# Performance work log

Hardware: AMD Instinct MI355X
Metric: run time of the kernel (lower is better)

Reference implementation:

```python
import jax, jax.numpy as jnp
import numpy as np

B, L, H, E = 4, 2048, 16, 64  # batch, seq, heads, head_dim (S=L, D=E)


def setup_inputs() -> dict:
    key = jax.random.key(0)
    kq, kk, kv = jax.random.split(key, 3)
    queries = jax.random.normal(kq, (B, L, H, E), dtype=jnp.float32)
    keys = jax.random.normal(kk, (B, L, H, E), dtype=jnp.float32)
    values = jax.random.normal(kv, (B, L, H, E), dtype=jnp.float32)
    return {"queries": queries, "keys": keys, "values": values}


def reference(queries, keys, values):
    Bq, Lq, Hq, Eq = queries.shape
    scale = 1.0 / float(np.sqrt(Eq))
    # scores: [B, H, L, S]
    scores = jnp.einsum('blhe,bshe->bhls', queries, keys)
    # causal mask: forbid attending to future positions (strict upper triangle)
    causal = jnp.triu(jnp.ones((Lq, Lq), dtype=bool), k=1)
    scores = jnp.where(causal[None, None, :, :], -jnp.inf, scores)
    A = jax.nn.softmax(scale * scores, axis=-1)  # dropout p=0 -> identity
    V = jnp.einsum('bhls,bshd->blhd', A, values)  # [B, L, H, D]
    return V
```

## Files before the change

kernel.cpp:

```cpp
#include <hip/hip_runtime.h>
#include <hip/hip_bf16.h>

typedef short bs8 __attribute__((ext_vector_type(8)));
typedef short bs4 __attribute__((ext_vector_type(4)));
typedef float f32x4 __attribute__((ext_vector_type(4)));
typedef float f32x16 __attribute__((ext_vector_type(16)));
typedef int i32x4 __attribute__((ext_vector_type(4)));

#define B_ 4
#define L_ 2048
#define H_ 16
#define E_ 64
#define KT_ 64
#define KSTR 72
#define SCSTR 68
#define NEG_INF (-1e30f)
#define SCALE_LOG2E (0.125f * 1.44269504088896340736f)

__device__ __forceinline__ short bf16of(float x) {
  __hip_bfloat16 h = __float2bfloat16(x);
  return *reinterpret_cast<short*>(&h);
}

__global__ __launch_bounds__(256) void prep(const float* __restrict__ K,
                                            const float* __restrict__ V,
                                            short* __restrict__ Kb,
                                            short* __restrict__ Vt) {
  __shared__ unsigned int lt[64 * 35];
  const int tid = threadIdx.x;
  if (blockIdx.x < 1024) {
    size_t base = (size_t)blockIdx.x * 256 + tid;
#pragma unroll
    for (int i = 0; i < 8; ++i) {
      size_t g = base + (size_t)i * 262144;
      int e4 = g & 15;
      int h  = (g >> 4) & 15;
      int s  = (g >> 8) & 2047;
      int b  = (int)(g >> 19);
      float4 v = *(const float4*)(K + g * 4);
      bs4 o;
      o.x = bf16of(v.x); o.y = bf16of(v.y); o.z = bf16of(v.z); o.w = bf16of(v.w);
      *(bs4*)(Kb + (((size_t)(b * 16 + h) * L_ + s) * E_ + e4 * 4)) = o;
    }
  } else {
    int vb = blockIdx.x - 1024;
    int st = vb & 31, bh = vb >> 5;
    int b = bh >> 4, h = bh & 15;
    int s0 = st * 64;
#pragma unroll
    for (int i = 0; i < 2; ++i) {
      int idx = i * 256 + tid;
      int sp = idx >> 4;
      int e4 = idx & 15;
      const float* p0 = V + (((size_t)b * L_ + s0 + 2 * sp) * H_ + h) * E_ + e4 * 4;
      float4 v0 = *(const float4*)p0;
      float4 v1 = *(const float4*)(p0 + H_ * E_);
      unsigned u;
      u = (unsigned short)bf16of(v0.x) | ((unsigned)(unsigned short)bf16of(v1.x) << 16);
      lt[(e4 * 4 + 0) * 35 + sp] = u;
      u = (unsigned short)bf16of(v0.y) | ((unsigned)(unsigned short)bf16of(v1.y) << 16);
      lt[(e4 * 4 + 1) * 35 + sp] = u;
      u = (unsigned short)bf16of(v0.z) | ((unsigned)(unsigned short)bf16of(v1.z) << 16);
      lt[(e4 * 4 + 2) * 35 + sp] = u;
      u = (unsigned short)bf16of(v0.w) | ((unsigned)(unsigned short)bf16of(v1.w) << 16);
      lt[(e4 * 4 + 3) * 35 + sp] = u;
    }
    __syncthreads();
#pragma unroll
    for (int i = 0; i < 2; ++i) {
      int idx = i * 256 + tid;
      int e  = idx >> 3;
      int s8 = idx & 7;
      uint4 o;
      o.x = lt[e * 35 + s8 * 4 + 0];
      o.y = lt[e * 35 + s8 * 4 + 1];
      o.z = lt[e * 35 + s8 * 4 + 2];
      o.w = lt[e * 35 + s8 * 4 + 3];
      *(uint4*)(Vt + ((size_t)bh * E_ + e) * L_ + s0 + 8 * s8) = o;
    }
  }
}

__global__ __launch_bounds__(256, 3) void flash_fwd(const float* __restrict__ Q,
                                                    const short* __restrict__ Kb,
                                                    const short* __restrict__ Vt,
                                                    float* __restrict__ O) {
  const int id  = blockIdx.x;
  const int xcd = id & 7;
  const int j   = id >> 3;
  const int qt  = 15 - (j & 15);
  const int bh  = xcd * 8 + (j >> 4);
  const int b = bh >> 4, h = bh & 15;
  const int tid = threadIdx.x;
  const int w = tid >> 6;
  const int lane = tid & 63;
  const int l32 = lane & 31;
  const int hh  = lane >> 5;
  const int h8  = hh * 8;

  __shared__ __align__(16) char smem[4 * 32 * SCSTR * 4];
  short* ldsK = (short*)smem;
  short* ldsV = (short*)(smem + KT_ * KSTR * 2);

  const short* KbBase = Kb + (size_t)bh * L_ * E_;
  const short* VtBase = Vt + (size_t)bh * E_ * L_;

  const int q0w = qt * 128 + w * 32;
  const int nkt = 2 * (qt + 1);

  const int sr = tid >> 3;
  const int sc8 = (tid & 7) * 8;

  bs8 aQ[4];
  {
    const float* qp = Q + (((size_t)b * L_ + q0w + l32) * H_ + h) * E_ + h8;
#pragma unroll
    for (int ks = 0; ks < 4; ++ks) {
      float4 f0 = *(const float4*)(qp + ks * 16);
      float4 f1 = *(const float4*)(qp + ks * 16 + 4);
      bs8 a;
      a[0] = bf16of(f0.x * SCALE_LOG2E); a[1] = bf16of(f0.y * SCALE_LOG2E);
      a[2] = bf16of(f0.z * SCALE_LOG2E); a[3] = bf16of(f0.w * SCALE_LOG2E);
      a[4] = bf16of(f1.x * SCALE_LOG2E); a[5] = bf16of(f1.y * SCALE_LOG2E);
      a[6] = bf16of(f1.z * SCALE_LOG2E); a[7] = bf16of(f1.w * SCALE_LOG2E);
      aQ[ks] = a;
    }
  }

  f32x16 accO[2];
#pragma unroll
  for (int d = 0; d < 2; ++d)
#pragma unroll
    for (int r = 0; r < 16; ++r) accO[d][r] = 0.f;
  float accL = 0.f;

  bs8 pfK[2], pfV[2];
#pragma unroll
  for (int i = 0; i < 2; ++i) {
    pfK[i] = *(const bs8*)(KbBase + (size_t)(sr + 32 * i) * E_ + sc8);
    pfV[i] = *(const bs8*)(VtBase + (size_t)(sr + 32 * i) * L_ + sc8);
  }

  for (int kt = 0; kt < nkt; ++kt) {
    const int k0 = kt * KT_;
    __syncthreads();
#pragma unroll
    for (int i = 0; i < 2; ++i) {
      *(bs8*)&ldsK[(sr + 32 * i) * KSTR + sc8] = pfK[i];
      *(bs8*)&ldsV[(sr + 32 * i) * KSTR + sc8] = pfV[i];
    }
    if (kt + 1 < nkt) {
      const int kn = k0 + KT_;
#pragma unroll
      for (int i = 0; i < 2; ++i) {
        pfK[i] = *(const bs8*)(KbBase + (size_t)(kn + sr + 32 * i) * E_ + sc8);
        pfV[i] = *(const bs8*)(VtBase + (size_t)(sr + 32 * i) * L_ + kn + sc8);
      }
    }
    __syncthreads();

    if (k0 > q0w + 31) continue;
    const bool diag = (k0 + KT_ - 1 > q0w);

    bs8 pB[2][2];
#pragma unroll
    for (int sub = 0; sub < 2; ++sub) {
      f32x16 cc;
#pragma unroll
      for (int r = 0; r < 16; ++r) cc[r] = 0.f;
#pragma unroll
      for (int ks = 0; ks < 4; ++ks) {
        bs8 aK = *(const bs8*)&ldsK[(sub * 32 + l32) * KSTR + ks * 16 + h8];
        cc = __builtin_amdgcn_mfma_f32_32x32x16_bf16(aK, aQ[ks], cc, 0, 0, 0);
      }
      if (diag) {
        const int qcol = q0w + l32;
#pragma unroll
        for (int r = 0; r < 16; ++r) {
          const int key = k0 + sub * 32 + ((r & 3) + 8 * (r >> 2) + 4 * hh);
          if (key > qcol) cc[r] = NEG_INF;
        }
      }
      float p[16];
#pragma unroll
      for (int r = 0; r < 16; ++r) p[r] = exp2f(cc[r]);
      accL += ((((p[0] + p[1]) + (p[2] + p[3])) + ((p[4] + p[5]) + (p[6] + p[7]))) +
               (((p[8] + p[9]) + (p[10] + p[11])) + ((p[12] + p[13]) + (p[14] + p[15]))));
      unsigned pk[8];
#pragma unroll
      for (int i = 0; i < 8; ++i)
        pk[i] = (unsigned)(unsigned short)bf16of(p[2 * i]) |
                ((unsigned)(unsigned short)bf16of(p[2 * i + 1]) << 16);
      unsigned w0 = pk[0], w2 = pk[2];
      asm("v_permlane32_swap_b32 %0, %1" : "+v"(w0), "+v"(w2));
      unsigned w1 = pk[1], w3 = pk[3];
      asm("v_permlane32_swap_b32 %0, %1" : "+v"(w1), "+v"(w3));
      unsigned w4 = pk[4], w6 = pk[6];
      asm("v_permlane32_swap_b32 %0, %1" : "+v"(w4), "+v"(w6));
      unsigned w5 = pk[5], w7 = pk[7];
      asm("v_permlane32_swap_b32 %0, %1" : "+v"(w5), "+v"(w7));
      i32x4 f0 = {(int)w0, (int)w1, (int)w2, (int)w3};
      i32x4 f1 = {(int)w4, (int)w5, (int)w6, (int)w7};
      pB[sub][0] = *(bs8*)&f0;
      pB[sub][1] = *(bs8*)&f1;
    }

#pragma unroll
    for (int dsub = 0; dsub < 2; ++dsub) {
#pragma unroll
      for (int sub = 0; sub < 2; ++sub) {
#pragma unroll
        for (int ks = 0; ks < 2; ++ks) {
          bs8 aV = *(const bs8*)&ldsV[(dsub * 32 + l32) * KSTR + sub * 32 + ks * 16 + h8];
          accO[dsub] = __builtin_amdgcn_mfma_f32_32x32x16_bf16(aV, pB[sub][ks], accO[dsub], 0, 0, 0);
        }
      }
    }
  }

  const float inv = 1.f / (accL + __shfl_xor(accL, 32, 64));

  __syncthreads();
  float* scb = (float*)(smem + w * (32 * SCSTR * 4));
#pragma unroll
  for (int dsub = 0; dsub < 2; ++dsub)
#pragma unroll
    for (int g = 0; g < 4; ++g) {
      f32x4 vv = {accO[dsub][4 * g + 0] * inv, accO[dsub][4 * g + 1] * inv,
                  accO[dsub][4 * g + 2] * inv, accO[dsub][4 * g + 3] * inv};
      *(f32x4*)&scb[(size_t)l32 * SCSTR + dsub * 32 + 8 * g + 4 * hh] = vv;
    }
#pragma unroll
  for (int jj = 0; jj < 8; ++jj) {
    const int qq = jj * 4 + (lane >> 4);
    const int d0 = (lane & 15) * 4;
    f32x4 ov = *(const f32x4*)&scb[(size_t)qq * SCSTR + d0];
    float* op = O + (((size_t)b * L_ + q0w + qq) * H_ + h) * E_ + d0;
    *(f32x4*)op = ov;
  }
}

extern "C" void kernel_launch(void* const* d_in, const int* in_sizes, int n_in,
                              void* d_out, int out_size, void* d_ws, size_t ws_size,
                              hipStream_t stream) {
  (void)in_sizes; (void)n_in; (void)out_size; (void)ws_size;
  const float* Q = (const float*)d_in[0];
  const float* K = (const float*)d_in[1];
  const float* V = (const float*)d_in[2];
  float* Out = (float*)d_out;
  short* Kb = (short*)d_ws;
  short* Vt = Kb + (size_t)B_ * H_ * L_ * E_;

  prep<<<1024 + 2048, 256, 0, stream>>>(K, V, Kb, Vt);
  flash_fwd<<<1024, 256, 0, stream>>>(Q, Kb, Vt, Out);
}
```

Baseline: 205.5 us.

## Split key tile across warp pairs and pair query tiles for causal load balance

Each block now handles two 64-row query tiles, p and 31-p, so every block does roughly equal causal work. Inside a block, the four warps form two query groups of 32 rows, and each pair of warps splits the 64-key tile in halves. Partial O and row-sum values from the two key halves are combined through LDS at the end. The change also raises launch bounds to 4 blocks per CU, aiming at better occupancy and tail balance, at the cost of an extra LDS reduction and more barriers per query tile.

New measurement: 201.3 us. 2.1% less time.

```diff
diff --git a/kernel.cpp b/kernel.cpp
--- a/kernel.cpp
+++ b/kernel.cpp
@@ -81,162 +81,181 @@
   }
 }
 
-__global__ __launch_bounds__(256, 3) void flash_fwd(const float* __restrict__ Q,
+__global__ __launch_bounds__(256, 4) void flash_fwd(const float* __restrict__ Q,
                                                     const short* __restrict__ Kb,
                                                     const short* __restrict__ Vt,
                                                     float* __restrict__ O) {
   const int id  = blockIdx.x;
   const int xcd = id & 7;
   const int j   = id >> 3;
-  const int qt  = 15 - (j & 15);
   const int bh  = xcd * 8 + (j >> 4);
+  const int p   = j & 15;
   const int b = bh >> 4, h = bh & 15;
   const int tid = threadIdx.x;
   const int w = tid >> 6;
+  const int g = w >> 1;
+  const int s = w & 1;
   const int lane = tid & 63;
   const int l32 = lane & 31;
   const int hh  = lane >> 5;
   const int h8  = hh * 8;
 
-  __shared__ __align__(16) char smem[4 * 32 * SCSTR * 4];
+  __shared__ __align__(16) char smem[18432];
   short* ldsK = (short*)smem;
   short* ldsV = (short*)(smem + KT_ * KSTR * 2);
+  float* scb  = (float*)smem;
 
   const short* KbBase = Kb + (size_t)bh * L_ * E_;
   const short* VtBase = Vt + (size_t)bh * E_ * L_;
 
-  const int q0w = qt * 128 + w * 32;
-  const int nkt = 2 * (qt + 1);
-
   const int sr = tid >> 3;
   const int sc8 = (tid & 7) * 8;
 
-  bs8 aQ[4];
-  {
-    const float* qp = Q + (((size_t)b * L_ + q0w + l32) * H_ + h) * E_ + h8;
-#pragma unroll
-    for (int ks = 0; ks < 4; ++ks) {
-      float4 f0 = *(const float4*)(qp + ks * 16);
-      float4 f1 = *(const float4*)(qp + ks * 16 + 4);
-      bs8 a;
-      a[0] = bf16of(f0.x * SCALE_LOG2E); a[1] = bf16of(f0.y * SCALE_LOG2E);
-      a[2] = bf16of(f0.z * SCALE_LOG2E); a[3] = bf16of(f0.w * SCALE_LOG2E);
-      a[4] = bf16of(f1.x * SCALE_LOG2E); a[5] = bf16of(f1.y * SCALE_LOG2E);
-      a[6] = bf16of(f1.z * SCALE_LOG2E); a[7] = bf16of(f1.w * SCALE_LOG2E);
-      aQ[ks] = a;
-    }
-  }
-
-  f32x16 accO[2];
-#pragma unroll
-  for (int d = 0; d < 2; ++d)
-#pragma unroll
-    for (int r = 0; r < 16; ++r) accO[d][r] = 0.f;
-  float accL = 0.f;
-
-  bs8 pfK[2], pfV[2];
-#pragma unroll
-  for (int i = 0; i < 2; ++i) {
-    pfK[i] = *(const bs8*)(KbBase + (size_t)(sr + 32 * i) * E_ + sc8);
-    pfV[i] = *(const bs8*)(VtBase + (size_t)(sr + 32 * i) * L_ + sc8);
-  }
-
-  for (int kt = 0; kt < nkt; ++kt) {
-    const int k0 = kt * KT_;
+  for (int phase = 0; phase < 2; ++phase) {
+    const int qt  = phase ? (31 - p) : p;
+    const int q0w = qt * 64 + 32 * s;
+    const int nkt = qt + 1;
+
+    bs8 aQ[4];
+    {
+      const float* qp = Q + (((size_t)b * L_ + q0w + l32) * H_ + h) * E_ + h8;
+#pragma unroll
+      for (int ks = 0; ks < 4; ++ks) {
+        float4 f0 = *(const float4*)(qp + ks * 16);
+        float4 f1 = *(const float4*)(qp + ks * 16 + 4);
+        bs8 a;
+        a[0] = bf16of(f0.x * SCALE_LOG2E); a[1] = bf16of(f0.y * SCALE_LOG2E);
+        a[2] = bf16of(f0.z * SCALE_LOG2E); a[3] = bf16of(f0.w * SCALE_LOG2E);
+        a[4] = bf16of(f1.x * SCALE_LOG2E); a[5] = bf16of(f1.y * SCALE_LOG2E);
+        a[6] = bf16of(f1.z * SCALE_LOG2E); a[7] = bf16of(f1.w * SCALE_LOG2E);
+        aQ[ks] = a;
+      }
+    }
+
+    f32x16 accO[2];
+#pragma unroll
+    for (int d = 0; d < 2; ++d)
+#pragma unroll
+      for (int r = 0; r < 16; ++r) accO[d][r] = 0.f;
+    float accL = 0.f;
+
+    bs8 pfK[2], pfV[2];
+#pragma unroll
+    for (int i = 0; i < 2; ++i) {
+      pfK[i] = *(const bs8*)(KbBase + (size_t)(sr + 32 * i) * E_ + sc8);
+      pfV[i] = *(const bs8*)(VtBase + (size_t)(sr + 32 * i) * L_ + sc8);
+    }
+
+    for (int kt = 0; kt < nkt; ++kt) {
+      const int k0 = kt * KT_;
+      __syncthreads();
+#pragma unroll
+      for (int i = 0; i < 2; ++i) {
+        *(bs8*)&ldsK[(sr + 32 * i) * KSTR + sc8] = pfK[i];
+        *(bs8*)&ldsV[(sr + 32 * i) * KSTR + sc8] = pfV[i];
+      }
+      if (kt + 1 < nkt) {
+        const int kn = k0 + KT_;
+#pragma unroll
+        for (int i = 0; i < 2; ++i) {
+          pfK[i] = *(const bs8*)(KbBase + (size_t)(kn + sr + 32 * i) * E_ + sc8);
+          pfV[i] = *(const bs8*)(VtBase + (size_t)(sr + 32 * i) * L_ + kn + sc8);
+        }
+      }
+      __syncthreads();
+
+      const int kb = k0 + 32 * g;
+      if (kb <= q0w + 31) {
+        const bool diag = (kb + 31 > q0w);
+
+        f32x16 cc;
+#pragma unroll
+        for (int r = 0; r < 16; ++r) cc[r] = 0.f;
+#pragma unroll
+        for (int ks = 0; ks < 4; ++ks) {
+          bs8 aK = *(const bs8*)&ldsK[(32 * g + l32) * KSTR + ks * 16 + h8];
+          cc = __builtin_amdgcn_mfma_f32_32x32x16_bf16(aK, aQ[ks], cc, 0, 0, 0);
+        }
+        if (diag) {
+          const int qcol = q0w + l32;
+#pragma unroll
+          for (int r = 0; r < 16; ++r) {
+            const int key = kb + ((r & 3) + 8 * (r >> 2) + 4 * hh);
+            if (key > qcol) cc[r] = NEG_INF;
+          }
+        }
+        float pv[16];
+#pragma unroll
+        for (int r = 0; r < 16; ++r) pv[r] = exp2f(cc[r]);
+        accL += ((((pv[0] + pv[1]) + (pv[2] + pv[3])) + ((pv[4] + pv[5]) + (pv[6] + pv[7]))) +
+                 (((pv[8] + pv[9]) + (pv[10] + pv[11])) + ((pv[12] + pv[13]) + (pv[14] + pv[15]))));
+        unsigned pk[8];
+#pragma unroll
+        for (int i = 0; i < 8; ++i)
+          pk[i] = (unsigned)(unsigned short)bf16of(pv[2 * i]) |
+                  ((unsigned)(unsigned short)bf16of(pv[2 * i + 1]) << 16);
+        unsigned w0 = pk[0], w2 = pk[2];
+        asm("v_permlane32_swap_b32 %0, %1" : "+v"(w0), "+v"(w2));
+        unsigned w1 = pk[1], w3 = pk[3];
+        asm("v_permlane32_swap_b32 %0, %1" : "+v"(w1), "+v"(w3));
+        unsigned w4 = pk[4], w6 = pk[6];
+        asm("v_permlane32_swap_b32 %0, %1" : "+v"(w4), "+v"(w6));
+        unsigned w5 = pk[5], w7 = pk[7];
+        asm("v_permlane32_swap_b32 %0, %1" : "+v"(w5), "+v"(w7));
+        i32x4 f0 = {(int)w0, (int)w1, (int)w2, (int)w3};
+        i32x4 f1 = {(int)w4, (int)w5, (int)w6, (int)w7};
+        bs8 pB0 = *(bs8*)&f0;
+        bs8 pB1 = *(bs8*)&f1;
+
+#pragma unroll
+        for (int dsub = 0; dsub < 2; ++dsub) {
+          bs8 aV0 = *(const bs8*)&ldsV[(dsub * 32 + l32) * KSTR + 32 * g + h8];
+          bs8 aV1 = *(const bs8*)&ldsV[(dsub * 32 + l32) * KSTR + 32 * g + 16 + h8];
+          accO[dsub] = __builtin_amdgcn_mfma_f32_32x32x16_bf16(aV0, pB0, accO[dsub], 0, 0, 0);
+          accO[dsub] = __builtin_amdgcn_mfma_f32_32x32x16_bf16(aV1, pB1, accO[dsub], 0, 0, 0);
+        }
+      }
+    }
+
+    const float Lf = accL + __shfl_xor(accL, 32, 64);
     __syncthreads();
-#pragma unroll
-    for (int i = 0; i < 2; ++i) {
-      *(bs8*)&ldsK[(sr + 32 * i) * KSTR + sc8] = pfK[i];
-      *(bs8*)&ldsV[(sr + 32 * i) * KSTR + sc8] = pfV[i];
-    }
-    if (kt + 1 < nkt) {
-      const int kn = k0 + KT_;
-#pragma unroll
-      for (int i = 0; i < 2; ++i) {
-        pfK[i] = *(const bs8*)(KbBase + (size_t)(kn + sr + 32 * i) * E_ + sc8);
-        pfV[i] = *(const bs8*)(VtBase + (size_t)(sr + 32 * i) * L_ + kn + sc8);
-      }
+    float* scbO = scb + s * (32 * SCSTR);
+    float* scbL = scb + 2 * (32 * SCSTR) + s * 32;
+    if (g == 1) {
+#pragma unroll
+      for (int dsub = 0; dsub < 2; ++dsub)
+#pragma unroll
+        for (int q4 = 0; q4 < 4; ++q4) {
+          f32x4 vv = {accO[dsub][4 * q4 + 0], accO[dsub][4 * q4 + 1],
+                      accO[dsub][4 * q4 + 2], accO[dsub][4 * q4 + 3]};
+          *(f32x4*)&scbO[(size_t)l32 * SCSTR + dsub * 32 + 8 * q4 + 4 * hh] = vv;
+        }
+      if (hh == 0) scbL[l32] = Lf;
     }
     __syncthreads();
-
-    if (k0 > q0w + 31) continue;
-    const bool diag = (k0 + KT_ - 1 > q0w);
-
-    bs8 pB[2][2];
-#pragma unroll
-    for (int sub = 0; sub < 2; ++sub) {
-      f32x16 cc;
-#pragma unroll
-      for (int r = 0; r < 16; ++r) cc[r] = 0.f;
-#pragma unroll
-      for (int ks = 0; ks < 4; ++ks) {
-        bs8 aK = *(const bs8*)&ldsK[(sub * 32 + l32) * KSTR + ks * 16 + h8];
-        cc = __builtin_amdgcn_mfma_f32_32x32x16_bf16(aK, aQ[ks], cc, 0, 0, 0);
-      }
-      if (diag) {
-        const int qcol = q0w + l32;
-#pragma unroll
-        for (int r = 0; r < 16; ++r) {
-          const int key = k0 + sub * 32 + ((r & 3) + 8 * (r >> 2) + 4 * hh);
-          if (key > qcol) cc[r] = NEG_INF;
-        }
-      }
-      float p[16];
-#pragma unroll
-      for (int r = 0; r < 16; ++r) p[r] = exp2f(cc[r]);
-      accL += ((((p[0] + p[1]) + (p[2] + p[3])) + ((p[4] + p[5]) + (p[6] + p[7]))) +
-               (((p[8] + p[9]) + (p[10] + p[11])) + ((p[12] + p[13]) + (p[14] + p[15]))));
-      unsigned pk[8];
-#pragma unroll
-      for (int i = 0; i < 8; ++i)
-        pk[i] = (unsigned)(unsigned short)bf16of(p[2 * i]) |
-                ((unsigned)(unsigned short)bf16of(p[2 * i + 1]) << 16);
-      unsigned w0 = pk[0], w2 = pk[2];
-      asm("v_permlane32_swap_b32 %0, %1" : "+v"(w0), "+v"(w2));
-      unsigned w1 = pk[1], w3 = pk[3];
-      asm("v_permlane32_swap_b32 %0, %1" : "+v"(w1), "+v"(w3));
-      unsigned w4 = pk[4], w6 = pk[6];
-      asm("v_permlane32_swap_b32 %0, %1" : "+v"(w4), "+v"(w6));
-      unsigned w5 = pk[5], w7 = pk[7];
-      asm("v_permlane32_swap_b32 %0, %1" : "+v"(w5), "+v"(w7));
-      i32x4 f0 = {(int)w0, (int)w1, (int)w2, (int)w3};
-      i32x4 f1 = {(int)w4, (int)w5, (int)w6, (int)w7};
-      pB[sub][0] = *(bs8*)&f0;
-      pB[sub][1] = *(bs8*)&f1;
-    }
-
-#pragma unroll
-    for (int dsub = 0; dsub < 2; ++dsub) {
-#pragma unroll
-      for (int sub = 0; sub < 2; ++sub) {
-#pragma unroll
-        for (int ks = 0; ks < 2; ++ks) {
-          bs8 aV = *(const bs8*)&ldsV[(dsub * 32 + l32) * KSTR + sub * 32 + ks * 16 + h8];
-          accO[dsub] = __builtin_amdgcn_mfma_f32_32x32x16_bf16(aV, pB[sub][ks], accO[dsub], 0, 0, 0);
-        }
-      }
-    }
-  }
-
-  const float inv = 1.f / (accL + __shfl_xor(accL, 32, 64));
-
-  __syncthreads();
-  float* scb = (float*)(smem + w * (32 * SCSTR * 4));
-#pragma unroll
-  for (int dsub = 0; dsub < 2; ++dsub)
-#pragma unroll
-    for (int g = 0; g < 4; ++g) {
-      f32x4 vv = {accO[dsub][4 * g + 0] * inv, accO[dsub][4 * g + 1] * inv,
-                  accO[dsub][4 * g + 2] * inv, accO[dsub][4 * g + 3] * inv};
-      *(f32x4*)&scb[(size_t)l32 * SCSTR + dsub * 32 + 8 * g + 4 * hh] = vv;
-    }
-#pragma unroll
-  for (int jj = 0; jj < 8; ++jj) {
-    const int qq = jj * 4 + (lane >> 4);
-    const int d0 = (lane & 15) * 4;
-    f32x4 ov = *(const f32x4*)&scb[(size_t)qq * SCSTR + d0];
-    float* op = O + (((size_t)b * L_ + q0w + qq) * H_ + h) * E_ + d0;
-    *(f32x4*)op = ov;
+    if (g == 0) {
+      const float inv = 1.f / (Lf + scbL[l32]);
+#pragma unroll
+      for (int dsub = 0; dsub < 2; ++dsub)
+#pragma unroll
+        for (int q4 = 0; q4 < 4; ++q4) {
+          float* ptr = &scbO[(size_t)l32 * SCSTR + dsub * 32 + 8 * q4 + 4 * hh];
+          f32x4 ov = *(const f32x4*)ptr;
+          f32x4 vv = {(accO[dsub][4 * q4 + 0] + ov.x) * inv,
+                      (accO[dsub][4 * q4 + 1] + ov.y) * inv,
+                      (accO[dsub][4 * q4 + 2] + ov.z) * inv,
+                      (accO[dsub][4 * q4 + 3] + ov.w) * inv};
+          *(f32x4*)ptr = vv;
+        }
+#pragma unroll
+      for (int jj = 0; jj < 8; ++jj) {
+        const int qq = jj * 4 + (lane >> 4);
+        const int d0 = (lane & 15) * 4;
+        f32x4 ov = *(const f32x4*)&scbO[(size_t)qq * SCSTR + d0];
+        float* op = O + (((size_t)b * L_ + qt * 64 + 32 * s + qq) * H_ + h) * E_ + d0;
+        *(f32x4*)op = ov;
+      }
+    }
   }
 }
 
```
